# Kernel tuning notes

Measured on AMD Instinct MI355X. Metric: run time of the kernel, lower is better.

## Reference

```python
import jax, jax.numpy as jnp
import numpy as np

SPATIAL_SHAPES = [(116, 200), (58, 100), (29, 50), (15, 25)]  # (H, W) per level
NUM_HEADS = 8
NUM_LEVELS = 4
NUM_POINTS = 8
NUM_Z = 4  # num_Z_anchors; NUM_POINTS must be divisible by NUM_Z
EMBED = 256


def _msda3d_forward(query, value, reference_points, w_off, b_off, w_attn, b_attn, w_val, b_val):
    bs, nq, _ = query.shape
    d = EMBED // NUM_HEADS
    # value projection -> (bs, num_value, heads, d)
    v = (value @ w_val + b_val).reshape(bs, -1, NUM_HEADS, d)
    # sampling offsets and attention weights from query
    off = (query @ w_off + b_off).reshape(bs, nq, NUM_HEADS, NUM_LEVELS, NUM_POINTS, 2)
    attn = (query @ w_attn + b_attn).reshape(bs, nq, NUM_HEADS, NUM_LEVELS * NUM_POINTS)
    attn = jax.nn.softmax(attn, axis=-1).reshape(bs, nq, NUM_HEADS, NUM_LEVELS, NUM_POINTS)
    # normalize offsets by (W, H) per level
    shapes = jnp.asarray(SPATIAL_SHAPES, dtype=query.dtype)  # (L,2) = (h,w)
    norm = jnp.stack([shapes[:, 1], shapes[:, 0]], axis=-1)  # (L,2) = (w,h)
    off = off / norm[None, None, None, :, None, :]
    # reference_points (bs,nq,Z,2) broadcast against offsets split over Z anchors
    p_per_z = NUM_POINTS // NUM_Z
    off = off.reshape(bs, nq, NUM_HEADS, NUM_LEVELS, p_per_z, NUM_Z, 2)
    loc = reference_points[:, :, None, None, None, :, :] + off
    loc = loc.reshape(bs, nq, NUM_HEADS, NUM_LEVELS, NUM_POINTS, 2)
    # per-level bilinear sampling (grid_sample, align_corners=False, zeros padding)
    out = jnp.zeros((bs, nq, NUM_HEADS, d), dtype=query.dtype)
    start = 0
    for lvl, (H, W) in enumerate(SPATIAL_SHAPES):
        v_l = v[:, start:start + H * W]  # (bs, H*W, heads, d)
        start += H * W
        locs = loc[:, :, :, lvl]  # (bs, nq, heads, P, 2) in [0,1]
        # grid = 2*loc-1, then unnormalize with align_corners=False: x = loc*W - 0.5
        x = locs[..., 0] * W - 0.5
        y = locs[..., 1] * H - 0.5
        x0 = jnp.floor(x)
        y0 = jnp.floor(y)
        lx = x - x0
        ly = y - y0
        x0i = x0.astype(jnp.int32)
        y0i = y0.astype(jnp.int32)
        samp = jnp.zeros((bs, nq, NUM_HEADS, NUM_POINTS, d), dtype=query.dtype)
        corners = ((0, 0, (1 - ly) * (1 - lx)), (0, 1, (1 - ly) * lx),
                   (1, 0, ly * (1 - lx)), (1, 1, ly * lx))
        for dy, dx, w in corners:
            xi = x0i + dx
            yi = y0i + dy
            valid = (xi >= 0) & (xi < W) & (yi >= 0) & (yi < H)
            idx = jnp.clip(yi, 0, H - 1) * W + jnp.clip(xi, 0, W - 1)  # (bs,nq,heads,P)
            # gather along flattened HW per (batch, head)
            idx2 = idx.transpose(0, 1, 3, 2).reshape(bs, nq * NUM_POINTS, NUM_HEADS)
            g = jnp.take_along_axis(v_l, idx2[..., None], axis=1)  # (bs, nq*P, heads, d)
            g = g.reshape(bs, nq, NUM_POINTS, NUM_HEADS, d).transpose(0, 1, 3, 2, 4)
            samp = samp + g * (w * valid.astype(query.dtype))[..., None]
        out = out + (samp * attn[:, :, :, lvl, :, None]).sum(axis=3)
    return out.reshape(bs, nq, EMBED)


def setup_inputs() -> dict:
    key = jax.random.key(0)
    ks = jax.random.split(key, 9)
    bs, nq = 6, 10000
    num_value = sum(h * w for h, w in SPATIAL_SHAPES)  # 30825
    return {
        "query": jax.random.normal(ks[0], (bs, nq, EMBED), jnp.float32),
        "value": jax.random.normal(ks[1], (bs, num_value, EMBED), jnp.float32),
        "reference_points": jax.random.uniform(ks[2], (bs, nq, NUM_Z, 2), jnp.float32),
        "w_off": jax.random.normal(ks[3], (EMBED, NUM_HEADS * NUM_LEVELS * NUM_POINTS * 2), jnp.float32) * 0.01,
        "b_off": jax.random.normal(ks[4], (NUM_HEADS * NUM_LEVELS * NUM_POINTS * 2,), jnp.float32) * 0.02,
        "w_attn": jax.random.normal(ks[5], (EMBED, NUM_HEADS * NUM_LEVELS * NUM_POINTS), jnp.float32) * 0.02,
        "b_attn": jnp.zeros((NUM_HEADS * NUM_LEVELS * NUM_POINTS,), jnp.float32),
        "w_val": jax.random.normal(ks[6], (EMBED, EMBED), jnp.float32) * 0.02,
        "b_val": jnp.zeros((EMBED,), jnp.float32),
    }


def reference(query, value, reference_points, w_off, b_off, w_attn, b_attn, w_val, b_val):
    return _msda3d_forward(query, value, reference_points, w_off, b_off, w_attn, b_attn, w_val, b_val)
```

## Files before the change

kernel.cpp:

```cpp
#include <hip/hip_runtime.h>
#include <hip/hip_bf16.h>

#define NQ 10000
#define BS 6
#define NV 30825

typedef __attribute__((ext_vector_type(8))) short bf16x8;
typedef __attribute__((ext_vector_type(4))) float f32x4;

__device__ __forceinline__ void gload_lds16(const void* g, void* l) {
  __builtin_amdgcn_global_load_lds(
      (const __attribute__((address_space(1))) unsigned int*)g,
      (__attribute__((address_space(3))) unsigned int*)l, 16, 0, 0);
}

__device__ __forceinline__ unsigned short bf_bits(float f) {
  __hip_bfloat16 h = __float2bfloat16(f);
  return *(unsigned short*)&h;
}

__global__ __launch_bounds__(256) void f32_to_bf16_kernel(
    const float* __restrict__ in, unsigned short* __restrict__ out, int n4) {
  int i = blockIdx.x * 256 + threadIdx.x;
  if (i >= n4) return;
  float4 v = ((const float4*)in)[i];
  ushort4 o;
  o.x = bf_bits(v.x); o.y = bf_bits(v.y); o.z = bf_bits(v.z); o.w = bf_bits(v.w);
  ((ushort4*)out)[i] = o;
}

__global__ __launch_bounds__(256) void prep_weights_kernel(
    const float* __restrict__ w_val, const float* __restrict__ w_off,
    const float* __restrict__ w_attn, const float* __restrict__ b_off,
    const float* __restrict__ b_attn, unsigned short* __restrict__ wvalT,
    unsigned short* __restrict__ wpackT, float* __restrict__ bpack) {
  int i = blockIdx.x * 256 + threadIdx.x;
  if (i < 65536) {
    int n = i >> 8, k = i & 255;
    wvalT[i] = bf_bits(w_val[k * 256 + n]);
  } else if (i < 65536 + 196608) {
    int j = i - 65536;
    int n = j >> 8, k = j & 255;
    float v = (n < 512) ? w_off[k * 512 + n] : w_attn[k * 256 + (n - 512)];
    wpackT[j] = bf_bits(v);
  } else if (i < 65536 + 196608 + 768) {
    int j = i - 262144;
    bpack[j] = (j < 512) ? b_off[j] : b_attn[j - 512];
  }
}

__global__ __launch_bounds__(256) void gemm_mfma_kernel(
    const unsigned short* __restrict__ A, const unsigned short* __restrict__ WT,
    const float* __restrict__ bias, unsigned short* __restrict__ C, int M, int N) {
  __shared__ short As[128 * 64];
  __shared__ short Bs[128 * 64];
  const int tid = threadIdx.x;
  const int wv = tid >> 6;
  const int lane = tid & 63;
  const int wr = wv >> 1, wc = wv & 1;
  const int m0 = blockIdx.x * 128;
  const int n0 = blockIdx.y * 128;

  f32x4 acc[4][4] = {};

  for (int kt = 0; kt < 4; ++kt) {
#pragma unroll
    for (int j = 0; j < 4; ++j) {
      int u = j * 256 + tid;
      int row = u >> 3;
      int kbyte = (u & 7) * 16;
      int ldsoff = (j * 256 + wv * 64) * 16;
      int gr = m0 + row; if (gr >= M) gr = M - 1;
      gload_lds16((const char*)A + (size_t)gr * 512 + kt * 128 + kbyte,
                  (char*)As + ldsoff);
      gload_lds16((const char*)WT + (size_t)(n0 + row) * 512 + kt * 128 + kbyte,
                  (char*)Bs + ldsoff);
    }
    __syncthreads();
#pragma unroll
    for (int kk = 0; kk < 2; ++kk) {
      bf16x8 af[4], bfr[4];
#pragma unroll
      for (int mi = 0; mi < 4; ++mi) {
        int off = (wr * 64 + mi * 16 + (lane & 15)) * 64 + kk * 32 + (lane >> 4) * 8;
        af[mi] = *(const bf16x8*)&As[off];
      }
#pragma unroll
      for (int ni = 0; ni < 4; ++ni) {
        int off = (wc * 64 + ni * 16 + (lane & 15)) * 64 + kk * 32 + (lane >> 4) * 8;
        bfr[ni] = *(const bf16x8*)&Bs[off];
      }
#pragma unroll
      for (int mi = 0; mi < 4; ++mi)
#pragma unroll
        for (int ni = 0; ni < 4; ++ni)
          acc[mi][ni] = __builtin_amdgcn_mfma_f32_16x16x32_bf16(
              af[mi], bfr[ni], acc[mi][ni], 0, 0, 0);
    }
    __syncthreads();
  }

  const int colb = n0 + wc * 64 + (lane & 15);
  float bvn[4];
#pragma unroll
  for (int ni = 0; ni < 4; ++ni) bvn[ni] = bias[colb + ni * 16];
#pragma unroll
  for (int mi = 0; mi < 4; ++mi) {
#pragma unroll
    for (int r = 0; r < 4; ++r) {
      int row = m0 + wr * 64 + mi * 16 + (lane >> 4) * 4 + r;
      if (row < M) {
#pragma unroll
        for (int ni = 0; ni < 4; ++ni)
          C[(size_t)row * N + colb + ni * 16] = bf_bits(acc[mi][ni][r] + bvn[ni]);
      }
    }
  }
}

__global__ __launch_bounds__(256) void msda_sample_kernel(
    const __hip_bfloat16* __restrict__ vproj,
    const __hip_bfloat16* __restrict__ C2,
    const float* __restrict__ ref,
    float* __restrict__ out) {
  const int bq = blockIdx.x;
  const int b = bq / NQ;
  const int tid = threadIdx.x;

  __shared__ float2 s_iw[256][4];

  {
    const int lp = tid & 31;
    const int l = lp >> 3, p = lp & 7, z = p & 3;
    const __hip_bfloat162* offp = (const __hip_bfloat162*)(C2 + (size_t)bq * 768);
    __hip_bfloat162 ob = offp[tid];
    float ox = __bfloat162float(ob.x), oy = __bfloat162float(ob.y);
    float logit = __bfloat162float(C2[(size_t)bq * 768 + 512 + tid]);

    float mx = logit;
#pragma unroll
    for (int m = 16; m >= 1; m >>= 1) mx = fmaxf(mx, __shfl_xor(mx, m, 32));
    float e = __expf(logit - mx);
    float s = e;
#pragma unroll
    for (int m = 16; m >= 1; m >>= 1) s += __shfl_xor(s, m, 32);
    float aw = e / s;

    float2 rz = *(const float2*)(ref + (size_t)bq * 8 + z * 2);
    const int W = 200 >> l;
    const int H = (l == 3) ? 15 : (116 >> l);
    const int base = (l == 0) ? 0 : (l == 1) ? 23200 : (l == 2) ? 29000 : 30450;

    float x = rz.x * (float)W + ox - 0.5f;
    float y = rz.y * (float)H + oy - 0.5f;
    float x0f = floorf(x), y0f = floorf(y);
    float lx = x - x0f, ly = y - y0f;
    int x0 = (int)x0f, y0 = (int)y0f;
    int x1 = x0 + 1, y1 = y0 + 1;

    float w00 = (1.f - ly) * (1.f - lx) * aw;
    float w01 = (1.f - ly) * lx * aw;
    float w10 = ly * (1.f - lx) * aw;
    float w11 = ly * lx * aw;

    if (!((x0 >= 0) & (x0 < W))) { w00 = 0.f; w10 = 0.f; }
    if (!((x1 >= 0) & (x1 < W))) { w01 = 0.f; w11 = 0.f; }
    if (!((y0 >= 0) & (y0 < H))) { w00 = 0.f; w01 = 0.f; }
    if (!((y1 >= 0) & (y1 < H))) { w10 = 0.f; w11 = 0.f; }

    int x0c = min(max(x0, 0), W - 1);
    int x1c = min(max(x1, 0), W - 1);
    int y0c = min(max(y0, 0), H - 1);
    int y1c = min(max(y1, 0), H - 1);

    s_iw[tid][0] = make_float2(__int_as_float(base + y0c * W + x0c), w00);
    s_iw[tid][1] = make_float2(__int_as_float(base + y0c * W + x1c), w01);
    s_iw[tid][2] = make_float2(__int_as_float(base + y1c * W + x0c), w10);
    s_iw[tid][3] = make_float2(__int_as_float(base + y1c * W + x1c), w11);
  }
  __syncthreads();

  const int h = tid >> 5;
  const int half = (tid >> 4) & 1;
  const int lane16 = tid & 15;
  const __hip_bfloat162* vb =
      (const __hip_bfloat162*)(vproj + (size_t)b * NV * 256 + h * 32 + lane16 * 2);
  float accx = 0.f, accy = 0.f;
  const int sbase = h * 32 + half * 16;
#pragma unroll 4
  for (int s = 0; s < 16; ++s) {
    int si = sbase + s;
#pragma unroll
    for (int corner = 0; corner < 4; ++corner) {
      float2 iw = s_iw[si][corner];
      int row = __float_as_int(iw.x);
      float w = iw.y;
      __hip_bfloat162 v = vb[(size_t)row * 128];
      accx = fmaf(w, __bfloat162float(v.x), accx);
      accy = fmaf(w, __bfloat162float(v.y), accy);
    }
  }
  accx += __shfl_xor(accx, 16);
  accy += __shfl_xor(accy, 16);
  if (!half) {
    *(float2*)(out + (size_t)bq * 256 + h * 32 + lane16 * 2) = make_float2(accx, accy);
  }
}

extern "C" void kernel_launch(void* const* d_in, const int* in_sizes, int n_in,
                              void* d_out, int out_size, void* d_ws, size_t ws_size,
                              hipStream_t stream) {
  const float* query  = (const float*)d_in[0];
  const float* value  = (const float*)d_in[1];
  const float* refp   = (const float*)d_in[2];
  const float* w_off  = (const float*)d_in[3];
  const float* b_off  = (const float*)d_in[4];
  const float* w_attn = (const float*)d_in[5];
  const float* b_attn = (const float*)d_in[6];
  const float* w_val  = (const float*)d_in[7];
  const float* b_val  = (const float*)d_in[8];
  float* out = (float*)d_out;

  char* ws = (char*)d_ws;
  unsigned short* vproj  = (unsigned short*)(ws);
  unsigned short* valb   = (unsigned short*)(ws + 94694400);
  unsigned short* C2     = (unsigned short*)(ws + 94694400);
  unsigned short* qb     = (unsigned short*)(ws + 189388800);
  unsigned short* wvalT  = (unsigned short*)(ws + 220108800);
  unsigned short* wpackT = (unsigned short*)(ws + 220239872);
  float*          bpack  = (float*)        (ws + 220633088);

  const int Mv = BS * NV;
  const int Mq = BS * NQ;

  prep_weights_kernel<<<1032, 256, 0, stream>>>(w_val, w_off, w_attn, b_off, b_attn,
                                                wvalT, wpackT, bpack);
  f32_to_bf16_kernel<<<(Mv * 64 + 255) / 256, 256, 0, stream>>>(value, valb, Mv * 64);
  f32_to_bf16_kernel<<<(Mq * 64 + 255) / 256, 256, 0, stream>>>(query, qb, Mq * 64);
  gemm_mfma_kernel<<<dim3((Mv + 127) / 128, 2), 256, 0, stream>>>(
      valb, wvalT, b_val, vproj, Mv, 256);
  gemm_mfma_kernel<<<dim3((Mq + 127) / 128, 6), 256, 0, stream>>>(
      qb, wpackT, bpack, C2, Mq, 768);
  msda_sample_kernel<<<BS * NQ, 256, 0, stream>>>(
      (const __hip_bfloat16*)vproj, (const __hip_bfloat16*)C2, refp, out);
}
```

Baseline: 423.1 us.

## Fuse fp32-to-bf16 conversion into GEMM loads and widen sampling gathers

The standalone fp32-to-bf16 conversion kernels for value and query are removed. The GEMM now reads fp32 activations directly, converts them in registers and stores bf16 into LDS, which avoids writing and re-reading the bf16 copies in global memory. Separately, the sampling kernel now has each lane gather 16 bytes (8 channels) per corner, with four lanes covering a head's 32 channels. Each 32-lane group splits the samples across lanes and reduces with shuffles, and index and weight tables move to a struct-of-arrays LDS layout. The cost is that the GEMM A-tile loads become synchronous register loads instead of async global-to-LDS loads, and the gather kernel does more shuffle reductions.

```diff
diff --git a/kernel.cpp b/kernel.cpp
--- a/kernel.cpp
+++ b/kernel.cpp
@@ -6,7 +6,9 @@
 #define NV 30825
 
 typedef __attribute__((ext_vector_type(8))) short bf16x8;
+typedef __attribute__((ext_vector_type(8))) unsigned short u16x8;
 typedef __attribute__((ext_vector_type(4))) float f32x4;
+typedef __attribute__((ext_vector_type(2))) float f32x2;
 
 __device__ __forceinline__ void gload_lds16(const void* g, void* l) {
   __builtin_amdgcn_global_load_lds(
@@ -17,16 +19,6 @@
 __device__ __forceinline__ unsigned short bf_bits(float f) {
   __hip_bfloat16 h = __float2bfloat16(f);
   return *(unsigned short*)&h;
-}
-
-__global__ __launch_bounds__(256) void f32_to_bf16_kernel(
-    const float* __restrict__ in, unsigned short* __restrict__ out, int n4) {
-  int i = blockIdx.x * 256 + threadIdx.x;
-  if (i >= n4) return;
-  float4 v = ((const float4*)in)[i];
-  ushort4 o;
-  o.x = bf_bits(v.x); o.y = bf_bits(v.y); o.z = bf_bits(v.z); o.w = bf_bits(v.w);
-  ((ushort4*)out)[i] = o;
 }
 
 __global__ __launch_bounds__(256) void prep_weights_kernel(
@@ -50,7 +42,7 @@
 }
 
 __global__ __launch_bounds__(256) void gemm_mfma_kernel(
-    const unsigned short* __restrict__ A, const unsigned short* __restrict__ WT,
+    const float* __restrict__ A, const unsigned short* __restrict__ WT,
     const float* __restrict__ bias, unsigned short* __restrict__ C, int M, int N) {
   __shared__ short As[128 * 64];
   __shared__ short Bs[128 * 64];
@@ -70,11 +62,19 @@
       int row = u >> 3;
       int kbyte = (u & 7) * 16;
       int ldsoff = (j * 256 + wv * 64) * 16;
-      int gr = m0 + row; if (gr >= M) gr = M - 1;
-      gload_lds16((const char*)A + (size_t)gr * 512 + kt * 128 + kbyte,
-                  (char*)As + ldsoff);
       gload_lds16((const char*)WT + (size_t)(n0 + row) * 512 + kt * 128 + kbyte,
                   (char*)Bs + ldsoff);
+    }
+#pragma unroll
+    for (int j = 0; j < 4; ++j) {
+      int u = j * 256 + tid;
+      int row = u >> 3, oct = u & 7;
+      int gr = m0 + row; if (gr >= M) gr = M - 1;
+      const float4* ap = (const float4*)(A + (size_t)gr * 256 + kt * 64 + oct * 8);
+      float4 a0 = ap[0], a1 = ap[1];
+      u16x8 pk = { bf_bits(a0.x), bf_bits(a0.y), bf_bits(a0.z), bf_bits(a0.w),
+                   bf_bits(a1.x), bf_bits(a1.y), bf_bits(a1.z), bf_bits(a1.w) };
+      *(u16x8*)&As[row * 64 + oct * 8] = pk;
     }
     __syncthreads();
 #pragma unroll
@@ -127,7 +127,8 @@
   const int b = bq / NQ;
   const int tid = threadIdx.x;
 
-  __shared__ float2 s_iw[256][4];
+  __shared__ int   s_idx[4][256];
+  __shared__ float s_w[4][256];
 
   {
     const int lp = tid & 31;
@@ -173,37 +174,52 @@
     int y0c = min(max(y0, 0), H - 1);
     int y1c = min(max(y1, 0), H - 1);
 
-    s_iw[tid][0] = make_float2(__int_as_float(base + y0c * W + x0c), w00);
-    s_iw[tid][1] = make_float2(__int_as_float(base + y0c * W + x1c), w01);
-    s_iw[tid][2] = make_float2(__int_as_float(base + y1c * W + x0c), w10);
-    s_iw[tid][3] = make_float2(__int_as_float(base + y1c * W + x1c), w11);
+    s_idx[0][tid] = base + y0c * W + x0c;  s_w[0][tid] = w00;
+    s_idx[1][tid] = base + y0c * W + x1c;  s_w[1][tid] = w01;
+    s_idx[2][tid] = base + y1c * W + x0c;  s_w[2][tid] = w10;
+    s_idx[3][tid] = base + y1c * W + x1c;  s_w[3][tid] = w11;
   }
   __syncthreads();
 
   const int h = tid >> 5;
-  const int half = (tid >> 4) & 1;
-  const int lane16 = tid & 15;
-  const __hip_bfloat162* vb =
-      (const __hip_bfloat162*)(vproj + (size_t)b * NV * 256 + h * 32 + lane16 * 2);
-  float accx = 0.f, accy = 0.f;
-  const int sbase = h * 32 + half * 16;
-#pragma unroll 4
-  for (int s = 0; s < 16; ++s) {
-    int si = sbase + s;
-#pragma unroll
-    for (int corner = 0; corner < 4; ++corner) {
-      float2 iw = s_iw[si][corner];
-      int row = __float_as_int(iw.x);
-      float w = iw.y;
-      __hip_bfloat162 v = vb[(size_t)row * 128];
-      accx = fmaf(w, __bfloat162float(v.x), accx);
-      accy = fmaf(w, __bfloat162float(v.y), accy);
-    }
-  }
-  accx += __shfl_xor(accx, 16);
-  accy += __shfl_xor(accy, 16);
-  if (!half) {
-    *(float2*)(out + (size_t)bq * 256 + h * 32 + lane16 * 2) = make_float2(accx, accy);
+  const int lane32 = tid & 31;
+  const int e = lane32 & 3;
+  const int sibase = tid & ~3;
+  const char* vrow = (const char*)vproj + (size_t)b * NV * 512 + h * 64 + e * 16;
+
+  f32x2 acc0 = {0.f, 0.f}, acc1 = {0.f, 0.f}, acc2 = {0.f, 0.f}, acc3 = {0.f, 0.f};
+#pragma unroll
+  for (int s = 0; s < 4; ++s) {
+    const int si = sibase + s;
+#pragma unroll
+    for (int c = 0; c < 4; ++c) {
+      int row = s_idx[c][si];
+      float w = s_w[c][si];
+      uint4 v = *(const uint4*)(vrow + (row << 9));
+      f32x2 wv = {w, w};
+      f32x2 p0 = {__uint_as_float(v.x << 16), __uint_as_float(v.x & 0xffff0000u)};
+      f32x2 p1 = {__uint_as_float(v.y << 16), __uint_as_float(v.y & 0xffff0000u)};
+      f32x2 p2 = {__uint_as_float(v.z << 16), __uint_as_float(v.z & 0xffff0000u)};
+      f32x2 p3 = {__uint_as_float(v.w << 16), __uint_as_float(v.w & 0xffff0000u)};
+      acc0 += wv * p0;
+      acc1 += wv * p1;
+      acc2 += wv * p2;
+      acc3 += wv * p3;
+    }
+  }
+
+#pragma unroll
+  for (int m = 4; m <= 16; m <<= 1) {
+    acc0.x += __shfl_xor(acc0.x, m, 32);  acc0.y += __shfl_xor(acc0.y, m, 32);
+    acc1.x += __shfl_xor(acc1.x, m, 32);  acc1.y += __shfl_xor(acc1.y, m, 32);
+    acc2.x += __shfl_xor(acc2.x, m, 32);  acc2.y += __shfl_xor(acc2.y, m, 32);
+    acc3.x += __shfl_xor(acc3.x, m, 32);  acc3.y += __shfl_xor(acc3.y, m, 32);
+  }
+
+  if (lane32 < 4) {
+    float4* op = (float4*)(out + (size_t)bq * 256 + h * 32 + e * 8);
+    op[0] = make_float4(acc0.x, acc0.y, acc1.x, acc1.y);
+    op[1] = make_float4(acc2.x, acc2.y, acc3.x, acc3.y);
   }
 }
 
@@ -223,24 +239,20 @@
 
   char* ws = (char*)d_ws;
   unsigned short* vproj  = (unsigned short*)(ws);
-  unsigned short* valb   = (unsigned short*)(ws + 94694400);
   unsigned short* C2     = (unsigned short*)(ws + 94694400);
-  unsigned short* qb     = (unsigned short*)(ws + 189388800);
-  unsigned short* wvalT  = (unsigned short*)(ws + 220108800);
-  unsigned short* wpackT = (unsigned short*)(ws + 220239872);
-  float*          bpack  = (float*)        (ws + 220633088);
+  unsigned short* wvalT  = (unsigned short*)(ws + 186854400);
+  unsigned short* wpackT = (unsigned short*)(ws + 186985472);
+  float*          bpack  = (float*)        (ws + 187378688);
 
   const int Mv = BS * NV;
   const int Mq = BS * NQ;
 
   prep_weights_kernel<<<1032, 256, 0, stream>>>(w_val, w_off, w_attn, b_off, b_attn,
                                                 wvalT, wpackT, bpack);
-  f32_to_bf16_kernel<<<(Mv * 64 + 255) / 256, 256, 0, stream>>>(value, valb, Mv * 64);
-  f32_to_bf16_kernel<<<(Mq * 64 + 255) / 256, 256, 0, stream>>>(query, qb, Mq * 64);
   gemm_mfma_kernel<<<dim3((Mv + 127) / 128, 2), 256, 0, stream>>>(
-      valb, wvalT, b_val, vproj, Mv, 256);
+      value, wvalT, b_val, vproj, Mv, 256);
   gemm_mfma_kernel<<<dim3((Mq + 127) / 128, 6), 256, 0, stream>>>(
-      qb, wpackT, bpack, C2, Mq, 768);
+      query, wpackT, bpack, C2, Mq, 768);
   msda_sample_kernel<<<BS * NQ, 256, 0, stream>>>(
       (const __hip_bfloat16*)vproj, (const __hip_bfloat16*)C2, refp, out);
 }
```

Result: slower. 452.7 us (+7.0%).
